# Kernel tuning notes

Measured on AMD Instinct MI355X. Metric: run time of the kernel, lower is better.

The kernel has to match this reference:

```python
import jax, jax.numpy as jnp
import numpy as np

LN_EPS = 1e-5
B, T, H = 32, 1024, 1024


def _layer_norm(v, g, b):
    m = v.mean(-1, keepdims=True)
    var = ((v - m) ** 2).mean(-1, keepdims=True)
    return (v - m) / jnp.sqrt(var + LN_EPS) * g + b


def setup_inputs() -> dict:
    key = jax.random.key(0)
    ks = jax.random.split(key, 10)
    s_t = 1.0 / np.sqrt(T)
    s_h = 1.0 / np.sqrt(H)
    return {
        "x": jax.random.normal(ks[0], (B, T, H), jnp.float32),
        # temporal MLP (square T x T, triangular-masked), torch Linear layout [out, in]
        "tw1": jax.random.uniform(ks[1], (T, T), jnp.float32, -s_t, s_t),
        "tb1": jax.random.uniform(ks[2], (T,), jnp.float32, -s_t, s_t),
        "tw2": jax.random.uniform(ks[3], (T, T), jnp.float32, -s_t, s_t),
        "tb2": jax.random.uniform(ks[4], (T,), jnp.float32, -s_t, s_t),
        # channel MLP (square H x H)
        "cw1": jax.random.uniform(ks[5], (H, H), jnp.float32, -s_h, s_h),
        "cb1": jax.random.uniform(ks[6], (H,), jnp.float32, -s_h, s_h),
        "cw2": jax.random.uniform(ks[7], (H, H), jnp.float32, -s_h, s_h),
        "cb2": jax.random.uniform(ks[8], (H,), jnp.float32, -s_h, s_h),
        # LayerNorm affine params
        "ln1_g": jnp.ones((H,), jnp.float32),
        "ln1_b": jnp.zeros((H,), jnp.float32),
        "ln2_g": jnp.ones((H,), jnp.float32),
        "ln2_b": jnp.zeros((H,), jnp.float32),
    }


def reference(x, tw1, tb1, tw2, tb2, cw1, cb1, cw2, cb2, ln1_g, ln1_b, ln2_g, ln2_b):
    t = tw1.shape[0]
    mask = jnp.tril(jnp.ones((t, t), x.dtype))  # diagonal=0: include self
    # temporal mixing: LN -> swap -> masked Linear -> GELU -> masked Linear -> swap
    y = _layer_norm(x, ln1_g, ln1_b)
    y = jnp.swapaxes(y, 1, 2)  # [B, H, T]
    y = y @ (mask * tw1).T + tb1
    y = jax.nn.gelu(y, approximate=False)
    y = y @ (mask * tw2).T + tb2
    y = jnp.swapaxes(y, 1, 2)  # [B, T, H]
    x = x + y
    # channel mixing: LN -> Linear -> GELU -> Linear
    y2 = _layer_norm(x, ln2_g, ln2_b)
    y2 = jax.nn.gelu(y2 @ cw1.T + cb1, approximate=False) @ cw2.T + cb2
    return x + y2
```

## Files before the change

### kernel.cpp

```cpp
#include <hip/hip_runtime.h>
#include <hip/hip_bf16.h>

#define BDIM 32
#define TDIM 1024
#define HDIM 1024
#define AS1 __attribute__((address_space(1)))
#define AS3 __attribute__((address_space(3)))

typedef __attribute__((ext_vector_type(8))) short short8;
typedef __attribute__((ext_vector_type(8))) unsigned short ushort8;
typedef __attribute__((ext_vector_type(4))) unsigned short u16x4;
typedef __attribute__((ext_vector_type(4))) float f32x4;

__device__ __forceinline__ float b2f(unsigned short h){ return __uint_as_float(((unsigned)h)<<16); }
__device__ __forceinline__ unsigned short f2b(float f){
  unsigned u = __float_as_uint(f);
  u += 0x7fffu + ((u>>16)&1u);
  return (unsigned short)(u>>16);
}
__device__ __forceinline__ float gelu_f(float v){ return 0.5f*v*(1.0f+erff(v*0.70710678118f)); }
__device__ __forceinline__ void stv(float* p, float v){ *p = v; }
__device__ __forceinline__ void stv(unsigned short* p, float v){ *p = f2b(v); }
__device__ __forceinline__ float ldr(float v){ return v; }
__device__ __forceinline__ float ldr(unsigned short v){ return b2f(v); }

__global__ void prep_weights(const float* __restrict__ w1, const float* __restrict__ w2,
                             const float* __restrict__ c1, const float* __restrict__ c2,
                             unsigned short* __restrict__ w1m, unsigned short* __restrict__ w2m,
                             unsigned short* __restrict__ c1b, unsigned short* __restrict__ c2b){
  int idx = blockIdx.x*blockDim.x + threadIdx.x;
  int e = idx*4;
  int i = e >> 10, j0 = e & 1023;
  f32x4 a = *(const f32x4*)(w1+e);
  f32x4 b = *(const f32x4*)(w2+e);
  f32x4 c = *(const f32x4*)(c1+e);
  f32x4 d = *(const f32x4*)(c2+e);
  u16x4 av, bv, cv, dv;
  #pragma unroll
  for (int q=0;q<4;++q){
    float am = (j0+q <= i) ? a[q] : 0.f;
    float bm = (j0+q <= i) ? b[q] : 0.f;
    av[q]=f2b(am); bv[q]=f2b(bm); cv[q]=f2b(c[q]); dv[q]=f2b(d[q]);
  }
  *(u16x4*)(w1m+e)=av; *(u16x4*)(w2m+e)=bv; *(u16x4*)(c1b+e)=cv; *(u16x4*)(c2b+e)=dv;
}

__global__ void ln_stats(const float* __restrict__ p, float* __restrict__ mean,
                         float* __restrict__ rstd){
  int wid = threadIdx.x>>6, lane = threadIdx.x&63;
  int row = blockIdx.x*4 + wid;
  const float* pr = p + (size_t)row*HDIM;
  float s=0.f, s2=0.f;
  #pragma unroll
  for (int it=0; it<4; ++it){
    f32x4 v = *(const f32x4*)(pr + it*256 + lane*4);
    #pragma unroll
    for (int c=0;c<4;++c){ s += v[c]; s2 += v[c]*v[c]; }
  }
  #pragma unroll
  for (int off=32; off>0; off>>=1){ s += __shfl_xor(s,off,64); s2 += __shfl_xor(s2,off,64); }
  if (lane==0){
    float m = s * (1.0f/HDIM);
    float var = s2 * (1.0f/HDIM) - m*m;
    mean[row]=m; rstd[row]=rsqrtf(var + 1e-5f);
  }
}

__global__ void ln_norm_transpose(const float* __restrict__ x, const float* __restrict__ mean,
                                  const float* __restrict__ rstd, const float* __restrict__ g,
                                  const float* __restrict__ bta, unsigned short* __restrict__ xnT){
  __shared__ float tile[64][65];
  int t0 = blockIdx.x*64, h0 = blockIdx.y*64, b = blockIdx.z;
  int tid = threadIdx.x;
  int rr = tid>>3, c8 = tid&7;
  size_t base = (size_t)b*TDIM*HDIM;
  #pragma unroll
  for (int p=0;p<2;++p){
    int r = rr + p*32;
    int trow = t0 + r;
    float m = mean[b*TDIM + trow], rs = rstd[b*TDIM + trow];
    f32x4 v0 = *(const f32x4*)(x + base + (size_t)trow*HDIM + h0 + c8*8);
    f32x4 v1 = *(const f32x4*)(x + base + (size_t)trow*HDIM + h0 + c8*8 + 4);
    #pragma unroll
    for (int c=0;c<4;++c){
      int h = c8*8+c;
      tile[r][h]   = (v0[c]-m)*rs*g[h0+h]   + bta[h0+h];
      tile[r][h+4] = (v1[c]-m)*rs*g[h0+h+4] + bta[h0+h+4];
    }
  }
  __syncthreads();
  #pragma unroll
  for (int p=0;p<2;++p){
    int hr = rr + p*32;
    ushort8 ov;
    #pragma unroll
    for (int c=0;c<8;++c) ov[c] = f2b(tile[c8*8+c][hr]);
    *(ushort8*)(xnT + base + (size_t)(h0+hr)*TDIM + t0 + c8*8) = ov;
  }
}

__global__ void ln_fused(const unsigned short* __restrict__ p, const float* __restrict__ g,
                         const float* __restrict__ bta, unsigned short* __restrict__ o){
  int wid = threadIdx.x>>6, lane = threadIdx.x&63;
  size_t row = (size_t)blockIdx.x*4 + wid;
  const unsigned short* pr = p + row*HDIM + lane*16;
  ushort8 v0 = *(const ushort8*)(pr);
  ushort8 v1 = *(const ushort8*)(pr+8);
  float f[16];
  float s=0.f, s2=0.f;
  #pragma unroll
  for (int c=0;c<8;++c){ f[c]=b2f(v0[c]); f[c+8]=b2f(v1[c]); }
  #pragma unroll
  for (int c=0;c<16;++c){ s += f[c]; s2 += f[c]*f[c]; }
  #pragma unroll
  for (int off=32; off>0; off>>=1){ s += __shfl_xor(s,off,64); s2 += __shfl_xor(s2,off,64); }
  float m = s * (1.0f/HDIM);
  float rs = rsqrtf(s2*(1.0f/HDIM) - m*m + 1e-5f);
  int h0 = lane*16;
  ushort8 o0, o1;
  #pragma unroll
  for (int c=0;c<8;++c){
    o0[c] = f2b((f[c]-m)*rs*g[h0+c] + bta[h0+c]);
    o1[c] = f2b((f[c+8]-m)*rs*g[h0+c+8] + bta[h0+c+8]);
  }
  *(ushort8*)(o + row*HDIM + h0) = o0;
  *(ushort8*)(o + row*HDIM + h0 + 8) = o1;
}

#define GATE(N) asm volatile("s_waitcnt vmcnt(" #N ")" ::: "memory")
#define BAR()   __builtin_amdgcn_s_barrier()

template<int MODE, typename CT, typename RT>
__global__ __launch_bounds__(512,1)
void gemmq(const unsigned short* __restrict__ act, const unsigned short* __restrict__ wgt,
           CT* __restrict__ C, const float* __restrict__ bias, const RT* __restrict__ resid){
  extern __shared__ char LDS[];
  const int bid = blockIdx.x;
  const int tile = (bid & 7)*64 + (bid >> 3);
  const int panel = tile >> 2;
  int inner = tile & 3;
  if constexpr (MODE==1 || MODE==2){ if (bid & 256) inner ^= 3; }
  const unsigned short *pa, *pb;
  size_t cbase; int rg0, cg0, kend;
  if constexpr (MODE==1){
    int b = panel>>2, mt = panel&3;
    pa = act + (size_t)b*1048576 + (size_t)mt*262144;
    pb = wgt + (size_t)inner*262144;
    kend = (inner+1)*256;
    cbase = (size_t)b*1048576; rg0 = mt*256; cg0 = inner*256;
  } else if constexpr (MODE==2){
    int b = panel>>2, nt = panel&3;
    pa = wgt + (size_t)inner*262144;
    pb = act + (size_t)b*1048576 + (size_t)nt*262144;
    kend = (inner+1)*256;
    cbase = (size_t)b*1048576; rg0 = inner*256; cg0 = nt*256;
  } else {
    pa = act + (size_t)panel*262144;
    pb = wgt + (size_t)inner*262144;
    kend = 1024;
    cbase = 0; rg0 = panel*256; cg0 = inner*256;
  }
  const int tid = threadIdx.x, lane = tid&63, wid = tid>>6;
  const int wrow = (wid>>2)*64;
  const int wcol = (wid&3)*32;
  const int l15 = lane&15, l4b = (lane>>4)<<4;
  f32x4 acc[8][4];
  #pragma unroll
  for (int i=0;i<8;++i)
    #pragma unroll
    for (int j=0;j<4;++j) acc[i][j] = (f32x4)(0.f);

  const int NT = kend>>6;

  auto STAGE = [&](int dt, int half, int st){
    const unsigned short* src = (half<2) ? pa : pb;
    const int rbase = (half&1)<<7;
    char* dst = LDS + ((dt&1)<<16) + (half<<14);
    const int k0 = st<<6;
    #pragma unroll
    for (int l=0;l<2;++l){
      int W = tid*16 + (l<<13);
      int r = W>>7;
      int cs = (W&127) ^ ((r&7)<<4);
      __builtin_amdgcn_global_load_lds(
        (const AS1 void*)(src + (size_t)(rbase+r)*1024 + k0 + (cs>>1)),
        (AS3 void*)(dst + W), 16, 0, 0);
    }
  };
  auto STG = [&](int tt, int half, int t_now){ STAGE(tt, half, tt<NT ? tt : t_now); };

  auto LDA = [&](int buf, int qa, int i, int s)->short8{
    int ra = wrow + i*16 + l15;
    int L = (ra<<7) + (((s<<6) + l4b) ^ ((ra&7)<<4));
    return *(const short8*)(LDS + (buf<<16) + (qa<<14) + L);
  };
  auto LDB = [&](int buf, int qb, int j, int s)->short8{
    int rb = wcol + j*16 + l15;
    int L = (rb<<7) + (((s<<6) + l4b) ^ ((rb&7)<<4));
    return *(const short8*)(LDS + (buf<<16) + ((2+qb)<<14) + L);
  };

  short8 aR[2][4], bR[2][2];

#define MFMAQ(qa,qb)                                                         \
  __builtin_amdgcn_s_setprio(1);                                             \
  _Pragma("unroll") for (int s=0;s<2;++s)                                    \
    _Pragma("unroll") for (int i=0;i<4;++i)                                  \
      _Pragma("unroll") for (int j=0;j<2;++j)                                \
        acc[(qa)*4+i][(qb)*2+j] = __builtin_amdgcn_mfma_f32_16x16x32_bf16(   \
            aR[s][i], bR[s][j], acc[(qa)*4+i][(qb)*2+j], 0,0,0);             \
  __builtin_amdgcn_s_setprio(0);

  STAGE(0,0,0); STAGE(0,2,0); STAGE(0,1,0); STAGE(0,3,0);
  STAGE(1,0, 1<NT ? 1 : 0);
  GATE(6); BAR();

  for (int t=0; t<NT; ++t){
    const int buf = t&1;
    #pragma unroll
    for (int s=0;s<2;++s){
      #pragma unroll
      for (int i=0;i<4;++i) aR[s][i] = LDA(buf,0,i,s);
      #pragma unroll
      for (int j=0;j<2;++j) bR[s][j] = LDB(buf,0,j,s);
    }
    STG(t+1, 2, t);
    GATE(4); BAR();
    MFMAQ(0,0)
    #pragma unroll
    for (int s=0;s<2;++s)
      #pragma unroll
      for (int j=0;j<2;++j) bR[s][j] = LDB(buf,1,j,s);
    STG(t+1, 1, t);
    MFMAQ(0,1)
    BAR();
    #pragma unroll
    for (int s=0;s<2;++s)
      #pragma unroll
      for (int i=0;i<4;++i) aR[s][i] = LDA(buf,1,i,s);
    STG(t+1, 3, t);
    MFMAQ(1,1)
    #pragma unroll
    for (int s=0;s<2;++s)
      #pragma unroll
      for (int j=0;j<2;++j) bR[s][j] = LDB(buf,0,j,s);
    STG(t+2, 0, t);
    MFMAQ(1,0)
    BAR();
  }
#undef MFMAQ

  #pragma unroll
  for (int I=0;I<8;++I){
    int rbase = rg0 + (I>>2)*128 + wrow + (I&3)*16 + ((lane>>4)<<2);
    #pragma unroll
    for (int J=0;J<4;++J){
      int cg = cg0 + (J>>1)*128 + wcol + (J&1)*16 + l15;
      float bn = (MODE!=2) ? bias[cg] : 0.f;
      #pragma unroll
      for (int r=0;r<4;++r){
        int rg = rbase + r;
        float v = acc[I][J][r];
        if (MODE==1 || MODE==3){ v += bn; v = gelu_f(v); }
        else if (MODE==2){ v += bias[rg]; v += ldr(resid[cbase + (size_t)rg*1024 + cg]); }
        else { v += bn; v += ldr(resid[cbase + (size_t)rg*1024 + cg]); }
        stv(&C[cbase + (size_t)rg*1024 + cg], v);
      }
    }
  }
}

extern "C" void kernel_launch(void* const* d_in, const int* in_sizes, int n_in,
                              void* d_out, int out_size, void* d_ws, size_t ws_size,
                              hipStream_t stream){
  const float* x    = (const float*)d_in[0];
  const float* tw1  = (const float*)d_in[1];
  const float* tb1  = (const float*)d_in[2];
  const float* tw2  = (const float*)d_in[3];
  const float* tb2  = (const float*)d_in[4];
  const float* cw1  = (const float*)d_in[5];
  const float* cb1  = (const float*)d_in[6];
  const float* cw2  = (const float*)d_in[7];
  const float* cb2  = (const float*)d_in[8];
  const float* g1   = (const float*)d_in[9];
  const float* bb1  = (const float*)d_in[10];
  const float* g2   = (const float*)d_in[11];
  const float* bb2  = (const float*)d_in[12];
  float* out = (float*)d_out;

  char* ws = (char*)d_ws;
  unsigned short* bufA = (unsigned short*)(ws);
  unsigned short* bufB = (unsigned short*)(ws + 67108864);
  unsigned short* xmid = (unsigned short*)(ws + 134217728);
  unsigned short* w1m  = (unsigned short*)(ws + 201326592);
  unsigned short* w2m  = (unsigned short*)(ws + 203423744);
  unsigned short* c1b  = (unsigned short*)(ws + 205520896);
  unsigned short* c2b  = (unsigned short*)(ws + 207618048);
  float* meanb = (float*)(ws + 209715200);
  float* rstdb = (float*)(ws + 209846272);

  prep_weights<<<1024,256,0,stream>>>(tw1,tw2,cw1,cw2,w1m,w2m,c1b,c2b);
  ln_stats<<<8192,256,0,stream>>>(x, meanb, rstdb);
  ln_norm_transpose<<<dim3(16,16,32),256,0,stream>>>(x, meanb, rstdb, g1, bb1, bufA);
  gemmq<1,unsigned short,float><<<512,512,131072,stream>>>(bufA, w1m, bufB, tb1, (const float*)nullptr);
  gemmq<2,unsigned short,float><<<512,512,131072,stream>>>(bufB, w2m, xmid, tb2, x);
  ln_fused<<<8192,256,0,stream>>>(xmid, g2, bb2, bufA);
  gemmq<3,unsigned short,unsigned short><<<512,512,131072,stream>>>(bufA, c1b, bufB, cb1, (const unsigned short*)nullptr);
  gemmq<4,float,unsigned short><<<512,512,131072,stream>>>(bufB, c2b, out, cb2, xmid);
}
```

Measured before the change: 477.2 us.

## Replace interleaved quarter-tile prefetch with whole-tile double buffering, unroll by two

The GEMM main loop used to stream the next k-tile into LDS one quarter at a time, interleaved with the MFMA quadrants, with several barriers per iteration. It now issues all four stage loads for the next tile at the start of each tile, waits on an older group, and then runs all four MFMA quadrants with a single trailing barrier. The loop is unrolled by two so the buffer index is a compile-time constant. This cuts barriers and address arithmetic per iteration, but a whole tile of loads is now in flight at once, which may expose more memory latency. It also assumes NT is even.

```diff
diff --git a/kernel.cpp b/kernel.cpp
--- a/kernel.cpp
+++ b/kernel.cpp
@@ -172,10 +172,10 @@
 
   const int NT = kend>>6;
 
-  auto STAGE = [&](int dt, int half, int st){
+  auto STAGE = [&](int dstbuf, int half, int st){
     const unsigned short* src = (half<2) ? pa : pb;
     const int rbase = (half&1)<<7;
-    char* dst = LDS + ((dt&1)<<16) + (half<<14);
+    char* dst = LDS + (dstbuf<<16) + (half<<14);
     const int k0 = st<<6;
     #pragma unroll
     for (int l=0;l<2;++l){
@@ -187,7 +187,6 @@
         (AS3 void*)(dst + W), 16, 0, 0);
     }
   };
-  auto STG = [&](int tt, int half, int t_now){ STAGE(tt, half, tt<NT ? tt : t_now); };
 
   auto LDA = [&](int buf, int qa, int i, int s)->short8{
     int ra = wrow + i*16 + l15;
@@ -211,44 +210,40 @@
             aR[s][i], bR[s][j], acc[(qa)*4+i][(qb)*2+j], 0,0,0);             \
   __builtin_amdgcn_s_setprio(0);
 
+#define TILE_BODY(BUF, TT)                                                   \
+  {                                                                          \
+    const int nsrc = ((TT)+1 < NT) ? (TT)+1 : (TT);                          \
+    STAGE(BUF^1, 0, nsrc); STAGE(BUF^1, 2, nsrc);                            \
+    STAGE(BUF^1, 1, nsrc); STAGE(BUF^1, 3, nsrc);                            \
+    GATE(8); BAR();                                                          \
+    _Pragma("unroll") for (int s=0;s<2;++s){                                 \
+      _Pragma("unroll") for (int i=0;i<4;++i) aR[s][i] = LDA(BUF,0,i,s);     \
+      _Pragma("unroll") for (int j=0;j<2;++j) bR[s][j] = LDB(BUF,0,j,s);     \
+    }                                                                        \
+    MFMAQ(0,0)                                                               \
+    _Pragma("unroll") for (int s=0;s<2;++s)                                  \
+      _Pragma("unroll") for (int j=0;j<2;++j) bR[s][j] = LDB(BUF,1,j,s);     \
+    MFMAQ(0,1)                                                               \
+    _Pragma("unroll") for (int s=0;s<2;++s)                                  \
+      _Pragma("unroll") for (int i=0;i<4;++i) aR[s][i] = LDA(BUF,1,i,s);     \
+    MFMAQ(1,1)                                                               \
+    _Pragma("unroll") for (int s=0;s<2;++s)                                  \
+      _Pragma("unroll") for (int j=0;j<2;++j) bR[s][j] = LDB(BUF,0,j,s);     \
+    MFMAQ(1,0)                                                               \
+    BAR();                                                                   \
+  }
+
   STAGE(0,0,0); STAGE(0,2,0); STAGE(0,1,0); STAGE(0,3,0);
-  STAGE(1,0, 1<NT ? 1 : 0);
-  GATE(6); BAR();
-
-  for (int t=0; t<NT; ++t){
-    const int buf = t&1;
-    #pragma unroll
-    for (int s=0;s<2;++s){
-      #pragma unroll
-      for (int i=0;i<4;++i) aR[s][i] = LDA(buf,0,i,s);
-      #pragma unroll
-      for (int j=0;j<2;++j) bR[s][j] = LDB(buf,0,j,s);
-    }
-    STG(t+1, 2, t);
-    GATE(4); BAR();
-    MFMAQ(0,0)
-    #pragma unroll
-    for (int s=0;s<2;++s)
-      #pragma unroll
-      for (int j=0;j<2;++j) bR[s][j] = LDB(buf,1,j,s);
-    STG(t+1, 1, t);
-    MFMAQ(0,1)
-    BAR();
-    #pragma unroll
-    for (int s=0;s<2;++s)
-      #pragma unroll
-      for (int i=0;i<4;++i) aR[s][i] = LDA(buf,1,i,s);
-    STG(t+1, 3, t);
-    MFMAQ(1,1)
-    #pragma unroll
-    for (int s=0;s<2;++s)
-      #pragma unroll
-      for (int j=0;j<2;++j) bR[s][j] = LDB(buf,0,j,s);
-    STG(t+2, 0, t);
-    MFMAQ(1,0)
-    BAR();
-  }
+  GATE(0); BAR();
+
+  for (int t=0; t<NT; t+=2){
+    TILE_BODY(0, t)
+    TILE_BODY(1, t+1)
+  }
+#undef TILE_BODY
 #undef MFMAQ
+
+  GATE(0);
 
   #pragma unroll
   for (int I=0;I<8;++I){
```

Measured after the change: 501.4 us. +5.1%, slower.
